# Kernel optimization log

Hardware: AMD Instinct MI355X
Metric: run time of the kernel (lower is better)

Reference implementation:

```python
import jax, jax.numpy as jnp
import numpy as np

P = 50000    # number of POIs (rows of HG_pu, size of square A)
U = 100000   # number of users (rows of HG_up)
NNZ = 1600000
D = 128      # emb_dim


def setup_inputs() -> dict:
    key = jax.random.key(0)
    ks = jax.random.split(key, 8)
    x = jax.random.normal(ks[0], (P, D), dtype=jnp.float32)
    e = jax.random.normal(ks[1], (P, D), dtype=jnp.float32)
    vals_up = jax.random.uniform(ks[2], (NNZ,), dtype=jnp.float32)
    vals_pu = jax.random.uniform(ks[3], (NNZ,), dtype=jnp.float32)
    rows_up = jax.random.randint(ks[4], (NNZ,), 0, U, dtype=jnp.int32)
    cols_up = jax.random.randint(ks[5], (NNZ,), 0, P, dtype=jnp.int32)
    rows_pu = jax.random.randint(ks[6], (NNZ,), 0, P, dtype=jnp.int32)
    cols_pu = jax.random.randint(ks[7], (NNZ,), 0, U, dtype=jnp.int32)
    return {"t": 0, "x": x, "e": e,
            "vals_up": vals_up, "vals_pu": vals_pu,
            "rows_up": rows_up, "cols_up": cols_up,
            "rows_pu": rows_pu, "cols_pu": cols_pu}


def _spmm(vals, rows, cols, dense, num_rows):
    # sparse [num_rows, *] @ dense -> [num_rows, D]
    gathered = vals[:, None] * dense[cols]          # [nnz, D]
    return jax.ops.segment_sum(gathered, rows, num_segments=num_rows)


def reference(t, x, e, vals_up, vals_pu, rows_up, cols_up, rows_pu, cols_pu):
    # A = HG_pu @ HG_up (never materialized);  out = (A - I) @ x + e
    y = _spmm(vals_up, rows_up, cols_up, x, U)      # HG_up @ x : [U, D]
    z = _spmm(vals_pu, rows_pu, cols_pu, y, P)      # HG_pu @ y : [P, D]
    return z - x + e                                # (A - I) x + e
```

## Files before the change

### kernel.cpp

```cpp
#include <hip/hip_runtime.h>

#define NP 50000
#define NU 100000
#define NNZ_C 1600000
#define NNZ2 (2 * NNZ_C)
#define DIM 128
#define NR_TOT (NU + NP)

#define RBSH 7
#define RB 128
#define NBK ((NR_TOT + RB - 1) / RB)
#define ITEMS 4096
#define NBLK ((NNZ2 + ITEMS - 1) / ITEMS)
#define CHUNK 4096
#define CPT (CHUNK / 256)

__device__ inline unsigned pack_bf16x2(float a, float b) {
    unsigned ia = __float_as_uint(a), ib = __float_as_uint(b);
    ia = (ia + 0x7FFFu + ((ia >> 16) & 1u)) >> 16;
    ib = (ib + 0x7FFFu + ((ib >> 16) & 1u)) >> 16;
    return ia | (ib << 16);
}

__device__ inline float dec_val(unsigned p) {
    return __uint_as_float((p & 0x7FFFu) << 16);
}

__global__ void cvt_bf16_kernel(const float* __restrict__ x,
                                unsigned* __restrict__ xh, int nwords) {
    int i = blockIdx.x * blockDim.x + threadIdx.x;
    if (i >= nwords) return;
    float2 v = ((const float2*)x)[i];
    xh[i] = pack_bf16x2(v.x, v.y);
}


__global__ void p1_hist_kernel(const int* __restrict__ rows_up,
                               const int* __restrict__ rows_pu,
                               int* __restrict__ hist_all) {
    __shared__ int h[NBK];
    for (int k = threadIdx.x; k < NBK; k += 256) h[k] = 0;
    __syncthreads();
    int base = blockIdx.x * ITEMS;
    for (int k = 0; k < ITEMS / 256; ++k) {
        int i = base + k * 256 + threadIdx.x;
        if (i >= NNZ2) break;
        int r = (i < NNZ_C) ? rows_up[i] : (NU + rows_pu[i - NNZ_C]);
        atomicAdd(&h[r >> RBSH], 1);
    }
    __syncthreads();
    for (int k = threadIdx.x; k < NBK; k += 256)
        hist_all[k * NBLK + blockIdx.x] = h[k];
}

__global__ void p1_scan_kernel(const int* __restrict__ hist_all,
                               int* __restrict__ base_all,
                               int* __restrict__ totals) {
    __shared__ int lds[512];
    int b = blockIdx.x;
    int t0 = threadIdx.x * 2;
    int e0 = (t0 < NBLK) ? hist_all[b * NBLK + t0] : 0;
    int e1 = (t0 + 1 < NBLK) ? hist_all[b * NBLK + t0 + 1] : 0;
    int a = e0 + e1;
    lds[threadIdx.x] = a;
    __syncthreads();
    for (int off = 1; off < 512; off <<= 1) {
        int t = (threadIdx.x >= (unsigned)off) ? lds[threadIdx.x - off] : 0;
        __syncthreads();
        lds[threadIdx.x] += t;
        __syncthreads();
    }
    int excl = lds[threadIdx.x] - a;
    if (t0 < NBLK) base_all[b * NBLK + t0] = excl;
    if (t0 + 1 < NBLK) base_all[b * NBLK + t0 + 1] = excl + e0;
    if (threadIdx.x == 511) totals[b] = lds[511];
}

__global__ void bucket_base_scan_kernel(const int* __restrict__ totals,
                                        int* __restrict__ bbase) {
    __shared__ int lds[1024];
    __shared__ int carry;
    if (threadIdx.x == 0) carry = 0;
    __syncthreads();
    for (int start = 0; start < NBK; start += 1024) {
        int i = start + threadIdx.x;
        int v = (i < NBK) ? totals[i] : 0;
        lds[threadIdx.x] = v;
        __syncthreads();
        for (int off = 1; off < 1024; off <<= 1) {
            int t = (threadIdx.x >= (unsigned)off) ? lds[threadIdx.x - off] : 0;
            __syncthreads();
            lds[threadIdx.x] += t;
            __syncthreads();
        }
        if (i < NBK) bbase[i] = carry + lds[threadIdx.x] - v;
        int tot = lds[1023];
        __syncthreads();
        if (threadIdx.x == 0) carry += tot;
        __syncthreads();
    }
    if (threadIdx.x == 0) bbase[NBK] = carry;
}

__global__ void p1_scatter_kernel(const float* __restrict__ vals_up,
                                  const float* __restrict__ vals_pu,
                                  const int* __restrict__ rows_up,
                                  const int* __restrict__ rows_pu,
                                  const int* __restrict__ cols_up,
                                  const int* __restrict__ cols_pu,
                                  const int* __restrict__ base_all,
                                  const int* __restrict__ bbase,
                                  unsigned* __restrict__ stag_pay,
                                  unsigned char* __restrict__ stag_row) {
    __shared__ unsigned spay[CHUNK];
    __shared__ unsigned sbr[CHUNK];
    __shared__ int h[NBK];
    __shared__ int cbase[NBK];
    __shared__ int off[NBK];
    __shared__ int tsum[256];

    int tid = threadIdx.x;
    int blk = blockIdx.x;
    for (int k = tid; k < NBK; k += 256) {
        cbase[k] = bbase[k] + base_all[k * NBLK + blk];
        h[k] = 0;
        off[k] = 0;
    }
    __syncthreads();

    int cbeg = blk * ITEMS;
    int cnt_items = NNZ2 - cbeg;
    if (cnt_items > CHUNK) cnt_items = CHUNK;

    unsigned rpay[CPT];
    int rrow[CPT];
    for (int k = 0; k < CPT; ++k) {
        int i = cbeg + k * 256 + tid;
        if (i < NNZ2) {
            int r, cc; float v;
            if (i < NNZ_C) { r = rows_up[i]; cc = cols_up[i]; v = vals_up[i]; }
            else { int q = i - NNZ_C; r = NU + rows_pu[q]; cc = cols_pu[q]; v = vals_pu[q]; }
            unsigned vb = __float_as_uint(v);
            unsigned vr = (vb + 0x7FFFu + ((vb >> 16) & 1u)) >> 16;
            rpay[k] = ((unsigned)cc << 15) | vr;
            rrow[k] = r;
            atomicAdd(&h[r >> RBSH], 1);
        } else {
            rrow[k] = -1;
        }
    }
    __syncthreads();

    {
        int s0 = tid * 5;
        int s1 = s0 + 5; if (s1 > NBK) s1 = NBK; if (s0 > NBK) s0 = NBK;
        int a = 0;
        for (int s = s0; s < s1; ++s) a += h[s];
        tsum[tid] = a;
        __syncthreads();
        for (int o = 1; o < 256; o <<= 1) {
            int t2 = (tid >= o) ? tsum[tid - o] : 0;
            __syncthreads();
            tsum[tid] += t2;
            __syncthreads();
        }
        int run = (tid == 0) ? 0 : tsum[tid - 1];
        for (int s = s0; s < s1; ++s) { int cc2 = h[s]; h[s] = run; run += cc2; }
    }
    __syncthreads();

    for (int k = 0; k < CPT; ++k) {
        if (rrow[k] < 0) continue;
        int b = rrow[k] >> RBSH;
        int lp = atomicAdd(&off[b], 1);
        int slot = h[b] + lp;
        spay[slot] = rpay[k];
        sbr[slot] = ((unsigned)b << 8) | (unsigned)(rrow[k] & (RB - 1));
    }
    __syncthreads();

    for (int s = tid; s < cnt_items; s += 256) {
        unsigned br = sbr[s];
        int b = (int)(br >> 8);
        int d = cbase[b] + (s - h[b]);
        stag_pay[d] = spay[s];
        stag_row[d] = (unsigned char)(br & 255u);
    }
}

__global__ void p2_finalize_kernel(const unsigned* __restrict__ stag_pay,
                                   const unsigned char* __restrict__ stag_row,
                                   const int* __restrict__ bbase,
                                   unsigned* __restrict__ packed,
                                   int* __restrict__ row_beg,
                                   int* __restrict__ row_cnt) {
    __shared__ int cnt[RB];
    __shared__ int scn[RB];
    __shared__ int cur[RB];
    int b = blockIdx.x;
    int beg = bbase[b], end = bbase[b + 1];
    if (threadIdx.x < RB) cnt[threadIdx.x] = 0;
    __syncthreads();
    for (int i = beg + threadIdx.x; i < end; i += 256)
        atomicAdd(&cnt[stag_row[i]], 1);
    __syncthreads();
    if (threadIdx.x < RB) scn[threadIdx.x] = cnt[threadIdx.x];
    __syncthreads();
    for (int off = 1; off < RB; off <<= 1) {
        int t = 0;
        if (threadIdx.x < RB && threadIdx.x >= (unsigned)off) t = scn[threadIdx.x - off];
        __syncthreads();
        if (threadIdx.x < RB) scn[threadIdx.x] += t;
        __syncthreads();
    }
    if (threadIdx.x < RB) {
        int excl = scn[threadIdx.x] - cnt[threadIdx.x];
        cur[threadIdx.x] = beg + excl;
        int rr = (b << RBSH) + threadIdx.x;
        if (rr < NR_TOT) { row_beg[rr] = beg + excl; row_cnt[rr] = cnt[threadIdx.x]; }
    }
    __syncthreads();
    for (int i = beg + threadIdx.x; i < end; i += 256) {
        int pos = atomicAdd(&cur[stag_row[i]], 1);
        packed[pos] = stag_pay[i];
    }
}


#define NZ_FMA(P, U)                                            \
    do {                                                         \
        acc.x += dec_val(P) * __uint_as_float((U) << 16);        \
        acc.y += dec_val(P) * __uint_as_float((U) & 0xFFFF0000u);\
    } while (0)

__device__ inline void gather_row(const unsigned* __restrict__ packed,
                                  const unsigned* __restrict__ src,
                                  int beg, int end, int lane, float2& acc) {
    beg = __builtin_amdgcn_readfirstlane(beg);
    end = __builtin_amdgcn_readfirstlane(end);
    int n = end - beg;
    const unsigned* prow = packed + beg;
    int j = 0;
    for (; j + 8 <= n; j += 8) {
        unsigned p0 = prow[j + 0];
        unsigned p1 = prow[j + 1];
        unsigned p2 = prow[j + 2];
        unsigned p3 = prow[j + 3];
        unsigned p4 = prow[j + 4];
        unsigned p5 = prow[j + 5];
        unsigned p6 = prow[j + 6];
        unsigned p7 = prow[j + 7];
        unsigned u0 = src[(p0 >> 15) * 64 + lane];
        unsigned u1 = src[(p1 >> 15) * 64 + lane];
        unsigned u2 = src[(p2 >> 15) * 64 + lane];
        unsigned u3 = src[(p3 >> 15) * 64 + lane];
        unsigned u4 = src[(p4 >> 15) * 64 + lane];
        unsigned u5 = src[(p5 >> 15) * 64 + lane];
        unsigned u6 = src[(p6 >> 15) * 64 + lane];
        unsigned u7 = src[(p7 >> 15) * 64 + lane];
        NZ_FMA(p0, u0); NZ_FMA(p1, u1); NZ_FMA(p2, u2); NZ_FMA(p3, u3);
        NZ_FMA(p4, u4); NZ_FMA(p5, u5); NZ_FMA(p6, u6); NZ_FMA(p7, u7);
    }
    for (; j + 4 <= n; j += 4) {
        unsigned p0 = prow[j + 0];
        unsigned p1 = prow[j + 1];
        unsigned p2 = prow[j + 2];
        unsigned p3 = prow[j + 3];
        unsigned u0 = src[(p0 >> 15) * 64 + lane];
        unsigned u1 = src[(p1 >> 15) * 64 + lane];
        unsigned u2 = src[(p2 >> 15) * 64 + lane];
        unsigned u3 = src[(p3 >> 15) * 64 + lane];
        NZ_FMA(p0, u0); NZ_FMA(p1, u1); NZ_FMA(p2, u2); NZ_FMA(p3, u3);
    }
    for (; j < n; ++j) {
        unsigned p = prow[j];
        unsigned u = src[(p >> 15) * 64 + lane];
        NZ_FMA(p, u);
    }
}

__global__ void spmm_gather_kernel(const int* __restrict__ row_beg,
                                   const int* __restrict__ row_cnt,
                                   const unsigned* __restrict__ packed,
                                   const unsigned* __restrict__ src,
                                   unsigned* __restrict__ dst) {
    int r = blockIdx.x * 4 + (threadIdx.x >> 6);
    if (r >= NU) return;
    int lane = threadIdx.x & 63;
    int beg = row_beg[r], end = beg + row_cnt[r];
    float2 acc = make_float2(0.f, 0.f);
    gather_row(packed, src, beg, end, lane, acc);
    dst[r * 64 + lane] = pack_bf16x2(acc.x, acc.y);
}

__global__ void spmm_gather_fused_kernel(const int* __restrict__ row_beg,
                                         const int* __restrict__ row_cnt,
                                         const unsigned* __restrict__ packed,
                                         const unsigned* __restrict__ src,
                                         const float* __restrict__ x,
                                         const float* __restrict__ e,
                                         float* __restrict__ out) {
    int r = blockIdx.x * 4 + (threadIdx.x >> 6);
    if (r >= NP) return;
    int lane = threadIdx.x & 63;
    int beg = row_beg[NU + r], end = beg + row_cnt[NU + r];
    float2 acc = make_float2(0.f, 0.f);
    gather_row(packed, src, beg, end, lane, acc);
    float2 xv = ((const float2*)(x + (size_t)r * DIM))[lane];
    float2 ev = ((const float2*)(e + (size_t)r * DIM))[lane];
    float2 o;
    o.x = acc.x - xv.x + ev.x;
    o.y = acc.y - xv.y + ev.y;
    ((float2*)(out + (size_t)r * DIM))[lane] = o;
}

extern "C" void kernel_launch(void* const* d_in, const int* in_sizes, int n_in,
                              void* d_out, int out_size, void* d_ws, size_t ws_size,
                              hipStream_t stream) {
    const float* x       = (const float*)d_in[1];
    const float* e       = (const float*)d_in[2];
    const float* vals_up = (const float*)d_in[3];
    const float* vals_pu = (const float*)d_in[4];
    const int*   rows_up = (const int*)d_in[5];
    const int*   cols_up = (const int*)d_in[6];
    const int*   rows_pu = (const int*)d_in[7];
    const int*   cols_pu = (const int*)d_in[8];
    float* out = (float*)d_out;

    char* ws = (char*)d_ws;
    unsigned* yh          = (unsigned*)(ws);
    unsigned* stag_pay    = (unsigned*)(ws);
    unsigned char* stag_row = (unsigned char*)(ws + 12800000);
    unsigned* xh     = (unsigned*)(ws + 25600000);
    unsigned* packed = (unsigned*)(ws + 38400000);
    int* hist_all    = (int*)(ws + 38400000);
    int* base_all    = (int*)(ws + 42065216);
    int* totals      = (int*)(ws + 54866496);
    int* bbase       = (int*)(ws + 54871184);
    int* row_beg     = (int*)(ws + 54875904);
    int* row_cnt     = (int*)(ws + 55475904);

    cvt_bf16_kernel<<<(NP * 64 + 255) / 256, 256, 0, stream>>>(x, xh, NP * 64);

    p1_hist_kernel<<<NBLK, 256, 0, stream>>>(rows_up, rows_pu, hist_all);
    p1_scan_kernel<<<NBK, 512, 0, stream>>>(hist_all, base_all, totals);
    bucket_base_scan_kernel<<<1, 1024, 0, stream>>>(totals, bbase);
    p1_scatter_kernel<<<NBLK, 256, 0, stream>>>(vals_up, vals_pu,
                                                rows_up, rows_pu,
                                                cols_up, cols_pu,
                                                base_all, bbase,
                                                stag_pay, stag_row);
    p2_finalize_kernel<<<NBK, 256, 0, stream>>>(stag_pay, stag_row, bbase,
                                                packed, row_beg, row_cnt);

    spmm_gather_kernel<<<(NU + 3) / 4, 256, 0, stream>>>(row_beg, row_cnt,
                                                         packed, xh, yh);

    spmm_gather_fused_kernel<<<(NP + 3) / 4, 256, 0, stream>>>(row_beg, row_cnt,
                                                               packed, yh,
                                                               x, e, out);
}
```

Baseline: 336.2 us.

## Merge bf16 convert into histogram kernel and use wave-shuffle scans

Fuses the x-to-bf16 conversion into the histogram kernel as extra blocks, removing one launch. Replaces the LDS Hillis-Steele scans in the block-scan, bucket-base scan and scatter kernels with 64-wide wavefront shuffle scans plus a small cross-wave combine, cutting many __syncthreads barriers. The scatter step now takes global destinations through atomic increments on per-bucket bases, encoded with the slot, which drops the later per-element base lookup. It also moves the base_all workspace offset. Wave64 is assumed, and the single-block bucket scan now handles at most 2048 buckets in one pass.

```diff
diff --git a/kernel.cpp b/kernel.cpp
--- a/kernel.cpp
+++ b/kernel.cpp
@@ -14,6 +14,8 @@
 #define NBLK ((NNZ2 + ITEMS - 1) / ITEMS)
 #define CHUNK 4096
 #define CPT (CHUNK / 256)
+#define CVT_NW (NP * 64)
+#define CVT_BLKS ((CVT_NW + 255) / 256)
 
 __device__ inline unsigned pack_bf16x2(float a, float b) {
     unsigned ia = __float_as_uint(a), ib = __float_as_uint(b);
@@ -26,80 +28,82 @@
     return __uint_as_float((p & 0x7FFFu) << 16);
 }
 
-__global__ void cvt_bf16_kernel(const float* __restrict__ x,
-                                unsigned* __restrict__ xh, int nwords) {
-    int i = blockIdx.x * blockDim.x + threadIdx.x;
-    if (i >= nwords) return;
-    float2 v = ((const float2*)x)[i];
-    xh[i] = pack_bf16x2(v.x, v.y);
-}
-
-
-__global__ void p1_hist_kernel(const int* __restrict__ rows_up,
-                               const int* __restrict__ rows_pu,
-                               int* __restrict__ hist_all) {
+__global__ void cvt_hist_kernel(const float* __restrict__ x,
+                                unsigned* __restrict__ xh,
+                                const int* __restrict__ rows_up,
+                                const int* __restrict__ rows_pu,
+                                int* __restrict__ hist_all) {
     __shared__ int h[NBK];
-    for (int k = threadIdx.x; k < NBK; k += 256) h[k] = 0;
-    __syncthreads();
-    int base = blockIdx.x * ITEMS;
-    for (int k = 0; k < ITEMS / 256; ++k) {
-        int i = base + k * 256 + threadIdx.x;
-        if (i >= NNZ2) break;
-        int r = (i < NNZ_C) ? rows_up[i] : (NU + rows_pu[i - NNZ_C]);
-        atomicAdd(&h[r >> RBSH], 1);
-    }
-    __syncthreads();
-    for (int k = threadIdx.x; k < NBK; k += 256)
-        hist_all[k * NBLK + blockIdx.x] = h[k];
+    if (blockIdx.x < NBLK) {
+        for (int k = threadIdx.x; k < NBK; k += 256) h[k] = 0;
+        __syncthreads();
+        int base = blockIdx.x * ITEMS;
+        for (int k = 0; k < ITEMS / 256; ++k) {
+            int i = base + k * 256 + threadIdx.x;
+            if (i >= NNZ2) break;
+            int r = (i < NNZ_C) ? rows_up[i] : (NU + rows_pu[i - NNZ_C]);
+            atomicAdd(&h[r >> RBSH], 1);
+        }
+        __syncthreads();
+        for (int k = threadIdx.x; k < NBK; k += 256)
+            hist_all[k * NBLK + blockIdx.x] = h[k];
+    } else {
+        int i = (blockIdx.x - NBLK) * 256 + threadIdx.x;
+        if (i < CVT_NW) {
+            float2 v = ((const float2*)x)[i];
+            xh[i] = pack_bf16x2(v.x, v.y);
+        }
+    }
 }
 
 __global__ void p1_scan_kernel(const int* __restrict__ hist_all,
                                int* __restrict__ base_all,
                                int* __restrict__ totals) {
-    __shared__ int lds[512];
+    __shared__ int ws[8];
     int b = blockIdx.x;
-    int t0 = threadIdx.x * 2;
+    int tid = threadIdx.x;
+    int t0 = tid * 2;
     int e0 = (t0 < NBLK) ? hist_all[b * NBLK + t0] : 0;
     int e1 = (t0 + 1 < NBLK) ? hist_all[b * NBLK + t0 + 1] : 0;
     int a = e0 + e1;
-    lds[threadIdx.x] = a;
-    __syncthreads();
-    for (int off = 1; off < 512; off <<= 1) {
-        int t = (threadIdx.x >= (unsigned)off) ? lds[threadIdx.x - off] : 0;
-        __syncthreads();
-        lds[threadIdx.x] += t;
-        __syncthreads();
-    }
-    int excl = lds[threadIdx.x] - a;
+    int lane = tid & 63, wid = tid >> 6;
+    int v = a;
+    for (int d = 1; d < 64; d <<= 1) {
+        int t = __shfl_up(v, d);
+        if (lane >= d) v += t;
+    }
+    if (lane == 63) ws[wid] = v;
+    __syncthreads();
+    int woff = 0;
+    for (int w = 0; w < wid; ++w) woff += ws[w];
+    int excl = woff + v - a;
     if (t0 < NBLK) base_all[b * NBLK + t0] = excl;
     if (t0 + 1 < NBLK) base_all[b * NBLK + t0 + 1] = excl + e0;
-    if (threadIdx.x == 511) totals[b] = lds[511];
+    if (tid == 511) totals[b] = woff + v;
 }
 
 __global__ void bucket_base_scan_kernel(const int* __restrict__ totals,
                                         int* __restrict__ bbase) {
-    __shared__ int lds[1024];
-    __shared__ int carry;
-    if (threadIdx.x == 0) carry = 0;
-    __syncthreads();
-    for (int start = 0; start < NBK; start += 1024) {
-        int i = start + threadIdx.x;
-        int v = (i < NBK) ? totals[i] : 0;
-        lds[threadIdx.x] = v;
-        __syncthreads();
-        for (int off = 1; off < 1024; off <<= 1) {
-            int t = (threadIdx.x >= (unsigned)off) ? lds[threadIdx.x - off] : 0;
-            __syncthreads();
-            lds[threadIdx.x] += t;
-            __syncthreads();
-        }
-        if (i < NBK) bbase[i] = carry + lds[threadIdx.x] - v;
-        int tot = lds[1023];
-        __syncthreads();
-        if (threadIdx.x == 0) carry += tot;
-        __syncthreads();
-    }
-    if (threadIdx.x == 0) bbase[NBK] = carry;
+    __shared__ int ws[16];
+    int tid = threadIdx.x;
+    int t0 = tid * 2;
+    int e0 = (t0 < NBK) ? totals[t0] : 0;
+    int e1 = (t0 + 1 < NBK) ? totals[t0 + 1] : 0;
+    int a = e0 + e1;
+    int lane = tid & 63, wid = tid >> 6;
+    int v = a;
+    for (int d = 1; d < 64; d <<= 1) {
+        int t = __shfl_up(v, d);
+        if (lane >= d) v += t;
+    }
+    if (lane == 63) ws[wid] = v;
+    __syncthreads();
+    int woff = 0;
+    for (int w = 0; w < wid; ++w) woff += ws[w];
+    int excl = woff + v - a;
+    if (t0 < NBK) bbase[t0] = excl;
+    if (t0 + 1 < NBK) bbase[t0 + 1] = excl + e0;
+    if (tid == 1023) bbase[NBK] = woff + v;
 }
 
 __global__ void p1_scatter_kernel(const float* __restrict__ vals_up,
@@ -113,19 +117,14 @@
                                   unsigned* __restrict__ stag_pay,
                                   unsigned char* __restrict__ stag_row) {
     __shared__ unsigned spay[CHUNK];
-    __shared__ unsigned sbr[CHUNK];
+    __shared__ unsigned sdr[CHUNK];
     __shared__ int h[NBK];
-    __shared__ int cbase[NBK];
-    __shared__ int off[NBK];
-    __shared__ int tsum[256];
+    __shared__ int cb[NBK];
+    __shared__ int ws[4];
 
     int tid = threadIdx.x;
     int blk = blockIdx.x;
-    for (int k = tid; k < NBK; k += 256) {
-        cbase[k] = bbase[k] + base_all[k * NBLK + blk];
-        h[k] = 0;
-        off[k] = 0;
-    }
+    for (int k = tid; k < NBK; k += 256) h[k] = 0;
     __syncthreads();
 
     int cbeg = blk * ITEMS;
@@ -149,6 +148,8 @@
             rrow[k] = -1;
         }
     }
+    for (int k = tid; k < NBK; k += 256)
+        cb[k] = bbase[k] + base_all[k * NBLK + blk];
     __syncthreads();
 
     {
@@ -156,35 +157,36 @@
         int s1 = s0 + 5; if (s1 > NBK) s1 = NBK; if (s0 > NBK) s0 = NBK;
         int a = 0;
         for (int s = s0; s < s1; ++s) a += h[s];
-        tsum[tid] = a;
-        __syncthreads();
-        for (int o = 1; o < 256; o <<= 1) {
-            int t2 = (tid >= o) ? tsum[tid - o] : 0;
-            __syncthreads();
-            tsum[tid] += t2;
-            __syncthreads();
+        int lane = tid & 63, wid = tid >> 6;
+        int v = a;
+        for (int d = 1; d < 64; d <<= 1) {
+            int t = __shfl_up(v, d);
+            if (lane >= d) v += t;
         }
-        int run = (tid == 0) ? 0 : tsum[tid - 1];
-        for (int s = s0; s < s1; ++s) { int cc2 = h[s]; h[s] = run; run += cc2; }
+        if (lane == 63) ws[wid] = v;
+        __syncthreads();
+        int woff = 0;
+        for (int w = 0; w < wid; ++w) woff += ws[w];
+        int run = woff + v - a;
+        for (int s = s0; s < s1; ++s) { int c = h[s]; h[s] = run; run += c; }
     }
     __syncthreads();
 
     for (int k = 0; k < CPT; ++k) {
         if (rrow[k] < 0) continue;
         int b = rrow[k] >> RBSH;
-        int lp = atomicAdd(&off[b], 1);
-        int slot = h[b] + lp;
+        int slot = atomicAdd(&h[b], 1);
+        int d = atomicAdd(&cb[b], 1);
         spay[slot] = rpay[k];
-        sbr[slot] = ((unsigned)b << 8) | (unsigned)(rrow[k] & (RB - 1));
+        sdr[slot] = ((unsigned)d << 7) | (unsigned)(rrow[k] & (RB - 1));
     }
     __syncthreads();
 
     for (int s = tid; s < cnt_items; s += 256) {
-        unsigned br = sbr[s];
-        int b = (int)(br >> 8);
-        int d = cbase[b] + (s - h[b]);
+        unsigned q = sdr[s];
+        int d = (int)(q >> 7);
         stag_pay[d] = spay[s];
-        stag_row[d] = (unsigned char)(br & 255u);
+        stag_row[d] = (unsigned char)(q & 127u);
     }
 }
 
@@ -334,15 +336,15 @@
     unsigned* xh     = (unsigned*)(ws + 25600000);
     unsigned* packed = (unsigned*)(ws + 38400000);
     int* hist_all    = (int*)(ws + 38400000);
-    int* base_all    = (int*)(ws + 42065216);
+    int* base_all    = (int*)(ws + 42066048);
     int* totals      = (int*)(ws + 54866496);
     int* bbase       = (int*)(ws + 54871184);
     int* row_beg     = (int*)(ws + 54875904);
     int* row_cnt     = (int*)(ws + 55475904);
 
-    cvt_bf16_kernel<<<(NP * 64 + 255) / 256, 256, 0, stream>>>(x, xh, NP * 64);
-
-    p1_hist_kernel<<<NBLK, 256, 0, stream>>>(rows_up, rows_pu, hist_all);
+    cvt_hist_kernel<<<NBLK + CVT_BLKS, 256, 0, stream>>>(x, xh, rows_up,
+                                                         rows_pu, hist_all);
+
     p1_scan_kernel<<<NBK, 512, 0, stream>>>(hist_all, base_all, totals);
     bucket_base_scan_kernel<<<1, 1024, 0, stream>>>(totals, bbase);
     p1_scatter_kernel<<<NBLK, 256, 0, stream>>>(vals_up, vals_pu,
```

Measured after the change: 325.9 us. -3.0%, faster.
